# Kernel tuning notes

Hardware: AMD Instinct MI355X
Metric: run time of the kernel (lower is better)

## Reference

```python
import jax, jax.numpy as jnp
import numpy as np

B, N1, N2 = 2, 2048, 8192
IN_F, OUT_F = 128, 64
ALPHA = 0.2
NEG = -9e15


def setup_inputs() -> dict:
    key = jax.random.key(0)
    ks = jax.random.split(key, 8)
    stdv = 1.0 / np.sqrt(OUT_F)
    x = jax.random.normal(ks[0], (B, N2, IN_F), dtype=jnp.float32)
    adj = (jax.random.uniform(ks[1], (B, N1, N2)) < 0.05).astype(jnp.float32)
    u = lambda k, shp: jax.random.uniform(k, shp, minval=-stdv, maxval=stdv, dtype=jnp.float32)
    W2 = u(ks[2], (IN_F, OUT_F))
    W3 = u(ks[3], (OUT_F, OUT_F))
    a = u(ks[4], (2 * OUT_F, 1))
    a2 = u(ks[5], (2 * OUT_F, 1))
    word_ctx = u(ks[6], (OUT_F,))
    return {"x": x, "adj": adj, "W2": W2, "W3": W3, "a": a, "a2": a2, "word_ctx": word_ctx}


def reference(x, adj, W2, W3, a, a2, word_ctx):
    F_out = W2.shape[1]
    x4 = jnp.einsum('bnf,fo->bno', x, W2)            # [B, N2, F] node features for attention
    mask = adj > 0                                     # [B, N1, N2]
    # --- stage 1: edge-level attention over member nodes (softmax over N2) ---
    # pair score = leakyrelu([word_ctx, x4_j] @ a); independent of hyperedge index i
    a_q, a_x = a[:F_out, 0], a[F_out:, 0]
    s1 = jax.nn.leaky_relu(jnp.dot(word_ctx, a_q) + x4 @ a_x, ALPHA)  # [B, N2]
    e1 = jnp.where(mask, s1[:, None, :], NEG)          # [B, N1, N2]
    att_edge = jax.nn.softmax(e1, axis=2)
    edge = jnp.einsum('bij,bjf->bif', att_edge, x4)    # [B, N1, F]
    edge4 = jnp.einsum('bif,fo->bio', edge, W3)        # [B, N1, F]
    # --- stage 2: node-level attention over incident hyperedges (softmax over N1) ---
    a2_x, a2_e = a2[:F_out, 0], a2[F_out:, 0]
    s2 = jax.nn.leaky_relu((edge4 @ a2_e)[:, :, None] + (x4 @ a2_x)[:, None, :], ALPHA)  # [B, N1, N2]
    e2 = jnp.where(mask, s2, NEG)
    att_node = jax.nn.softmax(jnp.transpose(e2, (0, 2, 1)), axis=2)  # [B, N2, N1]
    node = jnp.einsum('bji,bif->bjf', att_node, edge4)               # [B, N2, F]
    return node, edge
```

## Files before the change

kernel.cpp:

```cpp
#include <hip/hip_runtime.h>
#include <stdint.h>

#define NB 2
#define N1 2048
#define N2 8192
#define INF_ 128
#define F 64
#define ALPHA 0.2f
#define CAP_E 640
#define CAP_N 192

__device__ __forceinline__ float bf2f(unsigned short u) {
    return __uint_as_float((unsigned int)u << 16);
}
__device__ __forceinline__ unsigned short f2bf(float f) {
    unsigned int u = __float_as_uint(f);
    u += 0x7FFF + ((u >> 16) & 1);
    return (unsigned short)(u >> 16);
}

__global__ __launch_bounds__(256) void k_mask_csr(
    const float4* __restrict__ adj4, uint64_t* __restrict__ bits,
    uint16_t* __restrict__ idxE, int* __restrict__ cntE)
{
    __shared__ uint64_t sBits[128];
    __shared__ uint16_t sIdx[CAP_E];
    __shared__ int      sCnt[4];
    int tid  = threadIdx.x;
    int lane = tid & 63;
    int w    = tid >> 6;
    int row  = blockIdx.x;
    int b    = row >> 11;

    const float4* ar = adj4 + (size_t)row * (N2 / 4) + (size_t)w * 512 + lane;
    float4 v[8];
    #pragma unroll
    for (int it = 0; it < 8; ++it) v[it] = ar[it * 64];
    int cnt = 0;
    #pragma unroll
    for (int it = 0; it < 8; ++it) {
        unsigned long long m0 = __ballot(v[it].x != 0.0f);
        unsigned long long m1 = __ballot(v[it].y != 0.0f);
        unsigned long long m2 = __ballot(v[it].z != 0.0f);
        unsigned long long m3 = __ballot(v[it].w != 0.0f);
        if (lane == 0) {
            uint64_t* o = &sBits[w * 32 + it * 4];
            o[0] = m0; o[1] = m1; o[2] = m2; o[3] = m3;
        }
        cnt += (int)__popcll(m0) + (int)__popcll(m1)
             + (int)__popcll(m2) + (int)__popcll(m3);
    }
    if (lane == 0) sCnt[w] = cnt;
    __syncthreads();

    int c0 = sCnt[0], c1 = sCnt[1], c2 = sCnt[2], c3 = sCnt[3];
    int base = (w > 0 ? c0 : 0) + (w > 1 ? c1 : 0) + (w > 2 ? c2 : 0);
    int total = c0 + c1 + c2 + c3;
    uint64_t lmask = (1ull << lane) - 1;
    #pragma unroll
    for (int k = 0; k < 32; ++k) {
        int wi = w * 32 + k;
        uint64_t m = sBits[wi];
        if ((m >> lane) & 1) {
            int pos = base + (int)__popcll(m & lmask);
            sIdx[pos] = (uint16_t)(((wi >> 2) << 8) + (lane << 2) + (wi & 3));
        }
        base += (int)__popcll(m);
    }
    int n = total;
    int padded = (n + 15) & ~15;
    if (padded > CAP_E) padded = CAP_E;
    if (w == 3) {
        uint16_t sent = (uint16_t)((NB - b) * N2);
        if (n + lane < padded) sIdx[n + lane] = sent;
    }
    __syncthreads();

    uint64_t* bw = bits + (size_t)row * (N2 / 64);
    if (tid < 128) bw[tid] = sBits[tid];
    const uint32_t* s32 = (const uint32_t*)sIdx;
    uint32_t* o32 = (uint32_t*)(idxE + (size_t)row * CAP_E);
    for (int d = tid; 2 * d < padded; d += 256) o32[d] = s32[d];
    if (tid == 0) cntE[row] = n;
}

__global__ __launch_bounds__(512) void k_x4(
    const float* __restrict__ x, const float* __restrict__ W2,
    const float* __restrict__ a, const float* __restrict__ a2,
    const float* __restrict__ wctx,
    uint16_t* __restrict__ y16, float* __restrict__ w1, float* __restrict__ q)
{
    __shared__ float  w2s[INF_ * F];
    __shared__ float4 xs4[64 * 32];
    int tid  = threadIdx.x;
    int lane = tid & 63;
    int w    = tid >> 6;

    for (int idx = tid; idx < INF_ * F; idx += 512) w2s[idx] = W2[idx];
    if (blockIdx.x == 0) {
        if (tid < F) y16[(size_t)NB * N2 * F + tid] = 0;
        if (tid == 0) w1[NB * N2] = 0.f;
    }
    {
        const float4* xg4 = (const float4*)(x + (size_t)blockIdx.x * 64 * INF_);
        int r  = tid >> 3;
        int c0 = (tid & 7) * 4;
        #pragma unroll
        for (int i = 0; i < 4; ++i)
            xs4[r * 32 + c0 + i] = xg4[r * 32 + c0 + i];
    }
    float cpart = wctx[lane] * a[lane];
    #pragma unroll
    for (int s = 32; s; s >>= 1) cpart += __shfl_xor(cpart, s);
    float ax  = a[64 + lane];
    float a2x = a2[lane];
    __syncthreads();

    float acc[8] = {0.f, 0.f, 0.f, 0.f, 0.f, 0.f, 0.f, 0.f};
    for (int k4 = 0; k4 < 32; ++k4) {
        float wk0 = w2s[(4 * k4 + 0) * F + lane];
        float wk1 = w2s[(4 * k4 + 1) * F + lane];
        float wk2 = w2s[(4 * k4 + 2) * F + lane];
        float wk3 = w2s[(4 * k4 + 3) * F + lane];
        #pragma unroll
        for (int r = 0; r < 8; ++r) {
            float4 xv = xs4[(8 * w + r) * 32 + k4];
            acc[r] = fmaf(xv.x, wk0, acc[r]);
            acc[r] = fmaf(xv.y, wk1, acc[r]);
            acc[r] = fmaf(xv.z, wk2, acc[r]);
            acc[r] = fmaf(xv.w, wk3, acc[r]);
        }
    }
    int row0 = blockIdx.x * 64 + 8 * w;
    #pragma unroll
    for (int r = 0; r < 8; ++r) {
        float acc_ = acc[r];
        float r1 = acc_ * ax, r2 = acc_ * a2x;
        #pragma unroll
        for (int s = 32; s; s >>= 1) { r1 += __shfl_xor(r1, s); r2 += __shfl_xor(r2, s); }
        float s1 = cpart + r1;
        s1 = fmaxf(s1, ALPHA * s1);
        float wv1 = __expf(s1);
        y16[(size_t)(row0 + r) * F + lane] = f2bf(wv1 * acc_);
        if (lane == 0) { w1[row0 + r] = wv1; q[row0 + r] = r2; }
    }
}

union SU {
    float w3[F * F];
    struct {
        uint16_t idxn[64][194];
        int      pre[4][64];
        int      cnt[64];
    } t;
};

__global__ __launch_bounds__(256) void kB2(
    const uint64_t* __restrict__ bits,
    uint16_t* __restrict__ idxN, int* __restrict__ cntN,
    const uint16_t* __restrict__ idxE, const int* __restrict__ cntE,
    const uint16_t* __restrict__ y16, const float* __restrict__ w1,
    const float* __restrict__ W3, const float* __restrict__ a2,
    float* __restrict__ out_edge, uint16_t* __restrict__ e16, float* __restrict__ p)
{
    __shared__ SU su;
    int tid  = threadIdx.x;
    int lane = tid & 63;
    int w    = tid >> 6;

    if (blockIdx.x < 256) {
        int b  = blockIdx.x >> 7;
        int jw = blockIdx.x & 127;
        const uint64_t Mtab[6] = {0x00000000FFFFFFFFull, 0x0000FFFF0000FFFFull,
                                  0x00FF00FF00FF00FFull, 0x0F0F0F0F0F0F0F0Full,
                                  0x3333333333333333ull, 0x5555555555555555ull};
        uint64_t wd[8];
        #pragma unroll
        for (int t = 0; t < 8; ++t) {
            int ib = w * 8 + t;
            uint64_t xv = bits[((size_t)(b * N1 + ib * 64 + lane)) * (N2 / 64) + jw];
            #pragma unroll
            for (int st = 0; st < 6; ++st) {
                int s = 32 >> st;
                uint64_t M = Mtab[st];
                uint64_t yy = (uint64_t)__shfl_xor((unsigned long long)xv, s);
                xv = ((lane & s) == 0) ? ((xv & M) | ((yy & M) << s))
                                       : ((xv & ~M) | ((yy & ~M) >> s));
            }
            wd[t] = xv;
        }
        int myc = 0;
        #pragma unroll
        for (int t = 0; t < 8; ++t) myc += (int)__popcll(wd[t]);
        su.t.pre[w][lane] = myc;
        __syncthreads();
        int c0 = su.t.pre[0][lane], c1 = su.t.pre[1][lane];
        int c2 = su.t.pre[2][lane], c3 = su.t.pre[3][lane];
        int base = (w > 0 ? c0 : 0) + (w > 1 ? c1 : 0) + (w > 2 ? c2 : 0);
        int total = c0 + c1 + c2 + c3;
        int n = total < CAP_N ? total : CAP_N;
        if (w == 0) su.t.cnt[lane] = n;

        uint16_t* sr = su.t.idxn[lane];
        int off = base;
        #pragma unroll
        for (int t = 0; t < 8; ++t) {
            uint64_t m = wd[t];
            int ibase = (w * 8 + t) << 6;
            while (m) {
                int ii = __builtin_ctzll(m); m &= m - 1;
                if (off < CAP_N) sr[off] = (uint16_t)(ibase + ii);
                ++off;
            }
        }
        int jp = jw * 64 + lane;
        int j  = ((jp >> 8) << 8) + ((jp & 63) << 2) + ((jp >> 6) & 3);
        int rowOut = b * N2 + j;
        if (w == 3) {
            int padded = (n + 15) & ~15;
            if (padded > CAP_N) padded = CAP_N;
            uint16_t sent = (uint16_t)((NB - b) * N1);
            for (int o = n; o < padded; ++o) sr[o] = sent;
            cntN[rowOut] = n;
        }
        __syncthreads();
        int jbase = b * N2 + ((jw >> 2) << 8) + (jw & 3);
        for (int rr = 0; rr < 16; ++rr) {
            int r = w * 16 + rr;
            int n_r = su.t.cnt[r];
            int padded_r = (n_r + 15) & ~15;
            if (padded_r > CAP_N) padded_r = CAP_N;
            int rowOut_r = jbase + r * 4;
            uint32_t* dst = (uint32_t*)(idxN + (size_t)rowOut_r * CAP_N);
            const uint32_t* src = (const uint32_t*)su.t.idxn[r];
            for (int d = lane; 2 * d < padded_r; d += 64) dst[d] = src[d];
        }
    } else {
        for (int idx = tid; idx < F * F; idx += blockDim.x) su.w3[idx] = W3[idx];
        if (blockIdx.x == 256 && tid == 0) p[NB * N1] = -1e30f;
        __syncthreads();
        int g    = lane >> 4;
        int sub  = lane & 15;
        float a2e = a2[64 + lane];
        int row = ((blockIdx.x - 256) * 256 + tid) >> 6;
        if (row >= NB * N1) return;
        int b = row >> 11;
        const ushort4* yb = (const ushort4*)y16 + (size_t)b * N2 * 16;
        const float*   w1b = w1 + (size_t)b * N2;
        const uint16_t* ix = idxE + (size_t)row * CAP_E;
        int n = cntE[row];
        int padded = (n + 15) & ~15;
        if (padded > CAP_E) padded = CAP_E;
        float4 acc = make_float4(0.f, 0.f, 0.f, 0.f);
        float zl = 0.f, zl4 = 0.f;
        int t = 0;
        for (; t + 64 <= padded; t += 64) {
            int myj = ix[t + lane];
            zl += w1b[myj];
            #pragma unroll
            for (int s = 0; s < 16; ++s) {
                int jv = __shfl(myj, 4 * s + g);
                ushort4 v = yb[(size_t)jv * 16 + sub];
                acc.x += bf2f(v.x); acc.y += bf2f(v.y);
                acc.z += bf2f(v.z); acc.w += bf2f(v.w);
            }
        }
        for (; t < padded; t += 16) {
            int myj = ix[t + (lane & 15)];
            zl4 += w1b[myj];
            #pragma unroll
            for (int s = 0; s < 4; ++s) {
                int jv = __shfl(myj, 4 * s + g);
                ushort4 v = yb[(size_t)jv * 16 + sub];
                acc.x += bf2f(v.x); acc.y += bf2f(v.y);
                acc.z += bf2f(v.z); acc.w += bf2f(v.w);
            }
        }
        #pragma unroll
        for (int s2 = 16; s2 <= 32; s2 <<= 1) {
            acc.x += __shfl_xor(acc.x, s2);
            acc.y += __shfl_xor(acc.y, s2);
            acc.z += __shfl_xor(acc.z, s2);
            acc.w += __shfl_xor(acc.w, s2);
        }
        float zc = zl + 0.25f * zl4;
        #pragma unroll
        for (int s2 = 32; s2; s2 >>= 1) zc += __shfl_xor(zc, s2);
        float inv = 1.f / zc;
        float4 ev4 = make_float4(acc.x * inv, acc.y * inv, acc.z * inv, acc.w * inv);
        if (lane < 16) ((float4*)out_edge)[(size_t)row * 16 + sub] = ev4;
        float e0 = __shfl(ev4.x, lane >> 2);
        float e1 = __shfl(ev4.y, lane >> 2);
        float e2 = __shfl(ev4.z, lane >> 2);
        float e3 = __shfl(ev4.w, lane >> 2);
        int c = lane & 3;
        float ev = (c == 0) ? e0 : (c == 1) ? e1 : (c == 2) ? e2 : e3;
        float acc4 = 0.f;
        #pragma unroll 8
        for (int gg = 0; gg < 64; ++gg) acc4 += __shfl(ev, gg) * su.w3[gg * F + lane];
        e16[(size_t)row * F + lane] = f2bf(acc4);
        float r = acc4 * a2e;
        #pragma unroll
        for (int s2 = 32; s2; s2 >>= 1) r += __shfl_xor(r, s2);
        if (lane == 0) p[row] = r;
    }
}

__global__ __launch_bounds__(256) void kE(
    const uint16_t* __restrict__ idxN, const int* __restrict__ cntN,
    const uint16_t* __restrict__ e16, const float* __restrict__ p,
    const float* __restrict__ q, float* __restrict__ out_node)
{
    int lane = threadIdx.x & 63;
    int g    = lane >> 4;
    int sub  = lane & 15;
    int gw = (blockIdx.x * blockDim.x + threadIdx.x) >> 6;
    int nw = (gridDim.x * blockDim.x) >> 6;
    for (int row = gw; row < NB * N2; row += nw) {
        int b = row >> 13;
        const ushort4* eb = (const ushort4*)e16 + (size_t)b * N1 * 16;
        const float*   pb = p + b * N1;
        const uint16_t* ix = idxN + (size_t)row * CAP_N;
        float qj = q[row];
        int n = cntN[row];
        int padded = (n + 15) & ~15;
        if (padded > CAP_N) padded = CAP_N;
        float4 acc = make_float4(0.f, 0.f, 0.f, 0.f);
        float zl = 0.f, zl4 = 0.f;
        int t = 0;
        for (; t + 64 <= padded; t += 64) {
            int myi = ix[t + lane];
            float sc = pb[myi] + qj;
            sc = fmaxf(sc, ALPHA * sc);
            float wl = __expf(sc);
            zl += wl;
            #pragma unroll
            for (int s = 0; s < 16; ++s) {
                int iv   = __shfl(myi, 4 * s + g);
                float wv = __shfl(wl,  4 * s + g);
                ushort4 v = eb[(size_t)iv * 16 + sub];
                acc.x = fmaf(wv, bf2f(v.x), acc.x);
                acc.y = fmaf(wv, bf2f(v.y), acc.y);
                acc.z = fmaf(wv, bf2f(v.z), acc.z);
                acc.w = fmaf(wv, bf2f(v.w), acc.w);
            }
        }
        for (; t < padded; t += 16) {
            int myi = ix[t + (lane & 15)];
            float sc = pb[myi] + qj;
            sc = fmaxf(sc, ALPHA * sc);
            float wl = __expf(sc);
            zl4 += wl;
            #pragma unroll
            for (int s = 0; s < 4; ++s) {
                int iv   = __shfl(myi, 4 * s + g);
                float wv = __shfl(wl,  4 * s + g);
                ushort4 v = eb[(size_t)iv * 16 + sub];
                acc.x = fmaf(wv, bf2f(v.x), acc.x);
                acc.y = fmaf(wv, bf2f(v.y), acc.y);
                acc.z = fmaf(wv, bf2f(v.z), acc.z);
                acc.w = fmaf(wv, bf2f(v.w), acc.w);
            }
        }
        #pragma unroll
        for (int s2 = 16; s2 <= 32; s2 <<= 1) {
            acc.x += __shfl_xor(acc.x, s2);
            acc.y += __shfl_xor(acc.y, s2);
            acc.z += __shfl_xor(acc.z, s2);
            acc.w += __shfl_xor(acc.w, s2);
        }
        float zc = zl + 0.25f * zl4;
        #pragma unroll
        for (int s2 = 32; s2; s2 >>= 1) zc += __shfl_xor(zc, s2);
        float inv = 1.f / zc;
        if (lane < 16) {
            float4 o = make_float4(acc.x * inv, acc.y * inv, acc.z * inv, acc.w * inv);
            ((float4*)out_node)[(size_t)row * 16 + sub] = o;
        }
    }
}

extern "C" void kernel_launch(void* const* d_in, const int* in_sizes, int n_in,
                              void* d_out, int out_size, void* d_ws, size_t ws_size,
                              hipStream_t stream)
{
    const float* x    = (const float*)d_in[0];
    const float* adj  = (const float*)d_in[1];
    const float* W2   = (const float*)d_in[2];
    const float* W3   = (const float*)d_in[3];
    const float* a    = (const float*)d_in[4];
    const float* a2   = (const float*)d_in[5];
    const float* wctx = (const float*)d_in[6];

    float* out      = (float*)d_out;
    float* node_out = out;
    float* edge_out = out + (size_t)NB * N2 * F;

    char* basep = (char*)d_ws;
    size_t o = 0;
    uint16_t* y16 = (uint16_t*)(basep + o);
    o += (size_t)(NB * N2 + 1) * F * 2;        o = (o + 255) & ~(size_t)255;
    float* w1 = (float*)(basep + o);
    o += (size_t)(NB * N2 + 4) * 4;            o = (o + 255) & ~(size_t)255;
    float* q = (float*)(basep + o);
    o += (size_t)NB * N2 * 4;                  o = (o + 255) & ~(size_t)255;
    uint16_t* e16 = (uint16_t*)(basep + o);
    o += (size_t)(NB * N1 + 1) * F * 2;        o = (o + 255) & ~(size_t)255;
    float* p = (float*)(basep + o);
    o += (size_t)(NB * N1 + 4) * 4;            o = (o + 255) & ~(size_t)255;
    uint64_t* bits = (uint64_t*)(basep + o);
    o += (size_t)NB * N1 * (N2 / 64) * 8;
    int* cntE = (int*)(basep + o);             o += (size_t)NB * N1 * 4;
    int* cntN = (int*)(basep + o);             o += (size_t)NB * N2 * 4;
    uint16_t* idxE = (uint16_t*)(basep + o);   o += (size_t)NB * N1 * CAP_E * 2;
    uint16_t* idxN = (uint16_t*)(basep + o);

    hipLaunchKernelGGL(k_mask_csr, dim3(NB * N1), dim3(256), 0, stream,
                       (const float4*)adj, bits, idxE, cntE);
    hipLaunchKernelGGL(k_x4, dim3(NB * N2 / 64), dim3(512), 0, stream,
                       x, W2, a, a2, wctx, y16, w1, q);
    hipLaunchKernelGGL(kB2, dim3(1280), dim3(256), 0, stream,
                       bits, idxN, cntN, idxE, cntE, y16, w1, W3, a2,
                       edge_out, e16, p);
    hipLaunchKernelGGL(kE, dim3(4096), dim3(256), 0, stream,
                       idxN, cntN, e16, p, q, node_out);
}
```

Measured before the change: 97.36 us.

## Split each hyperedge row across four wavefronts with shared-memory reduction

The edge-aggregation branch of kB2 now gives each hyperedge row a whole 256-thread block instead of one wavefront. The four waves stride over the row's member list in 16-entry chunks, and their partial feature sums and softmax denominators are combined through shared memory. Wave 0 then applies the W3 projection and writes the outputs. This raises parallelism for long rows and shortens the per-row latency chain. The cost is four times as many blocks, a block-wide barrier, each block reloading W3 into shared memory, and three of the four waves sitting idle during the projection.

```diff
diff --git a/kernel.cpp b/kernel.cpp
--- a/kernel.cpp
+++ b/kernel.cpp
@@ -147,7 +147,11 @@
 }
 
 union SU {
-    float w3[F * F];
+    struct {
+        float  w3[F * F];
+        float4 red[4][16];
+        float  zred[4];
+    } d;
     struct {
         uint16_t idxn[64][194];
         int      pre[4][64];
@@ -236,36 +240,21 @@
             for (int d = lane; 2 * d < padded_r; d += 64) dst[d] = src[d];
         }
     } else {
-        for (int idx = tid; idx < F * F; idx += blockDim.x) su.w3[idx] = W3[idx];
+        for (int idx = tid; idx < F * F; idx += 256) su.d.w3[idx] = W3[idx];
         if (blockIdx.x == 256 && tid == 0) p[NB * N1] = -1e30f;
-        __syncthreads();
-        int g    = lane >> 4;
-        int sub  = lane & 15;
-        float a2e = a2[64 + lane];
-        int row = ((blockIdx.x - 256) * 256 + tid) >> 6;
-        if (row >= NB * N1) return;
+        int row = blockIdx.x - 256;
         int b = row >> 11;
         const ushort4* yb = (const ushort4*)y16 + (size_t)b * N2 * 16;
         const float*   w1b = w1 + (size_t)b * N2;
         const uint16_t* ix = idxE + (size_t)row * CAP_E;
+        int g    = lane >> 4;
+        int sub  = lane & 15;
         int n = cntE[row];
         int padded = (n + 15) & ~15;
         if (padded > CAP_E) padded = CAP_E;
         float4 acc = make_float4(0.f, 0.f, 0.f, 0.f);
-        float zl = 0.f, zl4 = 0.f;
-        int t = 0;
-        for (; t + 64 <= padded; t += 64) {
-            int myj = ix[t + lane];
-            zl += w1b[myj];
-            #pragma unroll
-            for (int s = 0; s < 16; ++s) {
-                int jv = __shfl(myj, 4 * s + g);
-                ushort4 v = yb[(size_t)jv * 16 + sub];
-                acc.x += bf2f(v.x); acc.y += bf2f(v.y);
-                acc.z += bf2f(v.z); acc.w += bf2f(v.w);
-            }
-        }
-        for (; t < padded; t += 16) {
+        float zl4 = 0.f;
+        for (int t = 16 * w; t < padded; t += 64) {
             int myj = ix[t + (lane & 15)];
             zl4 += w1b[myj];
             #pragma unroll
@@ -283,26 +272,40 @@
             acc.z += __shfl_xor(acc.z, s2);
             acc.w += __shfl_xor(acc.w, s2);
         }
-        float zc = zl + 0.25f * zl4;
+        float zc = 0.25f * zl4;
         #pragma unroll
         for (int s2 = 32; s2; s2 >>= 1) zc += __shfl_xor(zc, s2);
-        float inv = 1.f / zc;
-        float4 ev4 = make_float4(acc.x * inv, acc.y * inv, acc.z * inv, acc.w * inv);
-        if (lane < 16) ((float4*)out_edge)[(size_t)row * 16 + sub] = ev4;
-        float e0 = __shfl(ev4.x, lane >> 2);
-        float e1 = __shfl(ev4.y, lane >> 2);
-        float e2 = __shfl(ev4.z, lane >> 2);
-        float e3 = __shfl(ev4.w, lane >> 2);
-        int c = lane & 3;
-        float ev = (c == 0) ? e0 : (c == 1) ? e1 : (c == 2) ? e2 : e3;
-        float acc4 = 0.f;
-        #pragma unroll 8
-        for (int gg = 0; gg < 64; ++gg) acc4 += __shfl(ev, gg) * su.w3[gg * F + lane];
-        e16[(size_t)row * F + lane] = f2bf(acc4);
-        float r = acc4 * a2e;
-        #pragma unroll
-        for (int s2 = 32; s2; s2 >>= 1) r += __shfl_xor(r, s2);
-        if (lane == 0) p[row] = r;
+        if (lane < 16) su.d.red[w][sub] = acc;
+        if (lane == 0) su.d.zred[w] = zc;
+        __syncthreads();
+        if (w == 0) {
+            float4 A0 = su.d.red[0][sub], A1 = su.d.red[1][sub];
+            float4 A2 = su.d.red[2][sub], A3 = su.d.red[3][sub];
+            float4 As = make_float4((A0.x + A1.x) + (A2.x + A3.x),
+                                    (A0.y + A1.y) + (A2.y + A3.y),
+                                    (A0.z + A1.z) + (A2.z + A3.z),
+                                    (A0.w + A1.w) + (A2.w + A3.w));
+            float z = (su.d.zred[0] + su.d.zred[1]) + (su.d.zred[2] + su.d.zred[3]);
+            float inv = 1.f / z;
+            float4 ev4 = make_float4(As.x * inv, As.y * inv, As.z * inv, As.w * inv);
+            if (lane < 16) ((float4*)out_edge)[(size_t)row * 16 + sub] = ev4;
+            float e0 = __shfl(ev4.x, lane >> 2);
+            float e1 = __shfl(ev4.y, lane >> 2);
+            float e2 = __shfl(ev4.z, lane >> 2);
+            float e3 = __shfl(ev4.w, lane >> 2);
+            int c = lane & 3;
+            float ev = (c == 0) ? e0 : (c == 1) ? e1 : (c == 2) ? e2 : e3;
+            float a2e = a2[64 + lane];
+            float acc4 = 0.f;
+            #pragma unroll 8
+            for (int gg = 0; gg < 64; ++gg)
+                acc4 += __shfl(ev, gg) * su.d.w3[gg * F + lane];
+            e16[(size_t)row * F + lane] = f2bf(acc4);
+            float r = acc4 * a2e;
+            #pragma unroll
+            for (int s2 = 32; s2; s2 >>= 1) r += __shfl_xor(r, s2);
+            if (lane == 0) p[row] = r;
+        }
     }
 }
 
@@ -419,7 +422,7 @@
                        (const float4*)adj, bits, idxE, cntE);
     hipLaunchKernelGGL(k_x4, dim3(NB * N2 / 64), dim3(512), 0, stream,
                        x, W2, a, a2, wctx, y16, w1, q);
-    hipLaunchKernelGGL(kB2, dim3(1280), dim3(256), 0, stream,
+    hipLaunchKernelGGL(kB2, dim3(256 + NB * N1), dim3(256), 0, stream,
                        bits, idxN, cntN, idxE, cntE, y16, w1, W3, a2,
                        edge_out, e16, p);
     hipLaunchKernelGGL(kE, dim3(4096), dim3(256), 0, stream,
```

Measured after the change: 103.3 us. +6.1%, slower.

## Fuse node-CSR transpose into x4 kernel; split edge aggregation; widen gathers to 16B

Applied to the files above, without the earlier changes.

Moves the bit-matrix transpose that builds the node CSR out of the edge-aggregation kernel and into the x4 projection kernel, running it as extra 512-thread blocks there. Edge aggregation becomes its own kernel, so it no longer waits on the transpose work. Both gather loops (edge and node) now load 8 bf16 values per lane as uint4 instead of 4 as ushort4, halving the number of gather instructions and shuffles. Risks are changed occupancy from the larger shared-memory union, an extra launch boundary, and more registers per lane.

```diff
diff --git a/kernel.cpp b/kernel.cpp
--- a/kernel.cpp
+++ b/kernel.cpp
@@ -18,6 +18,8 @@
     u += 0x7FFF + ((u >> 16) & 1);
     return (unsigned short)(u >> 16);
 }
+__device__ __forceinline__ float blo(unsigned int d) { return __uint_as_float(d << 16); }
+__device__ __forceinline__ float bhi(unsigned int d) { return __uint_as_float(d & 0xFFFF0000u); }
 
 __global__ __launch_bounds__(256) void k_mask_csr(
     const float4* __restrict__ adj4, uint64_t* __restrict__ bits,
@@ -84,100 +86,88 @@
     if (tid == 0) cntE[row] = n;
 }
 
-__global__ __launch_bounds__(512) void k_x4(
+union XU {
+    struct { float w2s[INF_ * F]; float4 xs4[64 * 32]; } x;
+    struct {
+        uint16_t idxn[64][194];
+        int      pre[8][64];
+        int      cnt[64];
+    } t;
+};
+
+__global__ __launch_bounds__(512) void k_x4t(
     const float* __restrict__ x, const float* __restrict__ W2,
     const float* __restrict__ a, const float* __restrict__ a2,
     const float* __restrict__ wctx,
-    uint16_t* __restrict__ y16, float* __restrict__ w1, float* __restrict__ q)
+    uint16_t* __restrict__ y16, float* __restrict__ w1, float* __restrict__ q,
+    const uint64_t* __restrict__ bits,
+    uint16_t* __restrict__ idxN, int* __restrict__ cntN)
 {
-    __shared__ float  w2s[INF_ * F];
-    __shared__ float4 xs4[64 * 32];
+    __shared__ XU su;
     int tid  = threadIdx.x;
     int lane = tid & 63;
     int w    = tid >> 6;
 
-    for (int idx = tid; idx < INF_ * F; idx += 512) w2s[idx] = W2[idx];
-    if (blockIdx.x == 0) {
-        if (tid < F) y16[(size_t)NB * N2 * F + tid] = 0;
-        if (tid == 0) w1[NB * N2] = 0.f;
-    }
-    {
-        const float4* xg4 = (const float4*)(x + (size_t)blockIdx.x * 64 * INF_);
-        int r  = tid >> 3;
-        int c0 = (tid & 7) * 4;
-        #pragma unroll
-        for (int i = 0; i < 4; ++i)
-            xs4[r * 32 + c0 + i] = xg4[r * 32 + c0 + i];
-    }
-    float cpart = wctx[lane] * a[lane];
-    #pragma unroll
-    for (int s = 32; s; s >>= 1) cpart += __shfl_xor(cpart, s);
-    float ax  = a[64 + lane];
-    float a2x = a2[lane];
-    __syncthreads();
-
-    float acc[8] = {0.f, 0.f, 0.f, 0.f, 0.f, 0.f, 0.f, 0.f};
-    for (int k4 = 0; k4 < 32; ++k4) {
-        float wk0 = w2s[(4 * k4 + 0) * F + lane];
-        float wk1 = w2s[(4 * k4 + 1) * F + lane];
-        float wk2 = w2s[(4 * k4 + 2) * F + lane];
-        float wk3 = w2s[(4 * k4 + 3) * F + lane];
+    if (blockIdx.x < 256) {
+        for (int idx = tid; idx < INF_ * F; idx += 512) su.x.w2s[idx] = W2[idx];
+        if (blockIdx.x == 0) {
+            if (tid < F) y16[(size_t)NB * N2 * F + tid] = 0;
+            if (tid == 0) w1[NB * N2] = 0.f;
+        }
+        {
+            const float4* xg4 = (const float4*)(x + (size_t)blockIdx.x * 64 * INF_);
+            int r  = tid >> 3;
+            int c0 = (tid & 7) * 4;
+            #pragma unroll
+            for (int i = 0; i < 4; ++i)
+                su.x.xs4[r * 32 + c0 + i] = xg4[r * 32 + c0 + i];
+        }
+        float cpart = wctx[lane] * a[lane];
+        #pragma unroll
+        for (int s = 32; s; s >>= 1) cpart += __shfl_xor(cpart, s);
+        float ax  = a[64 + lane];
+        float a2x = a2[lane];
+        __syncthreads();
+
+        float acc[8] = {0.f, 0.f, 0.f, 0.f, 0.f, 0.f, 0.f, 0.f};
+        for (int k4 = 0; k4 < 32; ++k4) {
+            float wk0 = su.x.w2s[(4 * k4 + 0) * F + lane];
+            float wk1 = su.x.w2s[(4 * k4 + 1) * F + lane];
+            float wk2 = su.x.w2s[(4 * k4 + 2) * F + lane];
+            float wk3 = su.x.w2s[(4 * k4 + 3) * F + lane];
+            #pragma unroll
+            for (int r = 0; r < 8; ++r) {
+                float4 xv = su.x.xs4[(8 * w + r) * 32 + k4];
+                acc[r] = fmaf(xv.x, wk0, acc[r]);
+                acc[r] = fmaf(xv.y, wk1, acc[r]);
+                acc[r] = fmaf(xv.z, wk2, acc[r]);
+                acc[r] = fmaf(xv.w, wk3, acc[r]);
+            }
+        }
+        int row0 = blockIdx.x * 64 + 8 * w;
         #pragma unroll
         for (int r = 0; r < 8; ++r) {
-            float4 xv = xs4[(8 * w + r) * 32 + k4];
-            acc[r] = fmaf(xv.x, wk0, acc[r]);
-            acc[r] = fmaf(xv.y, wk1, acc[r]);
-            acc[r] = fmaf(xv.z, wk2, acc[r]);
-            acc[r] = fmaf(xv.w, wk3, acc[r]);
-        }
-    }
-    int row0 = blockIdx.x * 64 + 8 * w;
-    #pragma unroll
-    for (int r = 0; r < 8; ++r) {
-        float acc_ = acc[r];
-        float r1 = acc_ * ax, r2 = acc_ * a2x;
-        #pragma unroll
-        for (int s = 32; s; s >>= 1) { r1 += __shfl_xor(r1, s); r2 += __shfl_xor(r2, s); }
-        float s1 = cpart + r1;
-        s1 = fmaxf(s1, ALPHA * s1);
-        float wv1 = __expf(s1);
-        y16[(size_t)(row0 + r) * F + lane] = f2bf(wv1 * acc_);
-        if (lane == 0) { w1[row0 + r] = wv1; q[row0 + r] = r2; }
-    }
-}
-
-union SU {
-    float w3[F * F];
-    struct {
-        uint16_t idxn[64][194];
-        int      pre[4][64];
-        int      cnt[64];
-    } t;
-};
-
-__global__ __launch_bounds__(256) void kB2(
-    const uint64_t* __restrict__ bits,
-    uint16_t* __restrict__ idxN, int* __restrict__ cntN,
-    const uint16_t* __restrict__ idxE, const int* __restrict__ cntE,
-    const uint16_t* __restrict__ y16, const float* __restrict__ w1,
-    const float* __restrict__ W3, const float* __restrict__ a2,
-    float* __restrict__ out_edge, uint16_t* __restrict__ e16, float* __restrict__ p)
-{
-    __shared__ SU su;
-    int tid  = threadIdx.x;
-    int lane = tid & 63;
-    int w    = tid >> 6;
-
-    if (blockIdx.x < 256) {
-        int b  = blockIdx.x >> 7;
-        int jw = blockIdx.x & 127;
+            float acc_ = acc[r];
+            float r1 = acc_ * ax, r2 = acc_ * a2x;
+            #pragma unroll
+            for (int s = 32; s; s >>= 1) { r1 += __shfl_xor(r1, s); r2 += __shfl_xor(r2, s); }
+            float s1 = cpart + r1;
+            s1 = fmaxf(s1, ALPHA * s1);
+            float wv1 = __expf(s1);
+            y16[(size_t)(row0 + r) * F + lane] = f2bf(wv1 * acc_);
+            if (lane == 0) { w1[row0 + r] = wv1; q[row0 + r] = r2; }
+        }
+    } else {
+        int blk = blockIdx.x - 256;
+        int b  = blk >> 7;
+        int jw = blk & 127;
         const uint64_t Mtab[6] = {0x00000000FFFFFFFFull, 0x0000FFFF0000FFFFull,
                                   0x00FF00FF00FF00FFull, 0x0F0F0F0F0F0F0F0Full,
                                   0x3333333333333333ull, 0x5555555555555555ull};
-        uint64_t wd[8];
-        #pragma unroll
-        for (int t = 0; t < 8; ++t) {
-            int ib = w * 8 + t;
+        uint64_t wd[4];
+        #pragma unroll
+        for (int t = 0; t < 4; ++t) {
+            int ib = w * 4 + t;
             uint64_t xv = bits[((size_t)(b * N1 + ib * 64 + lane)) * (N2 / 64) + jw];
             #pragma unroll
             for (int st = 0; st < 6; ++st) {
@@ -191,22 +181,25 @@
         }
         int myc = 0;
         #pragma unroll
-        for (int t = 0; t < 8; ++t) myc += (int)__popcll(wd[t]);
+        for (int t = 0; t < 4; ++t) myc += (int)__popcll(wd[t]);
         su.t.pre[w][lane] = myc;
         __syncthreads();
-        int c0 = su.t.pre[0][lane], c1 = su.t.pre[1][lane];
-        int c2 = su.t.pre[2][lane], c3 = su.t.pre[3][lane];
-        int base = (w > 0 ? c0 : 0) + (w > 1 ? c1 : 0) + (w > 2 ? c2 : 0);
-        int total = c0 + c1 + c2 + c3;
+        int base = 0, total = 0;
+        #pragma unroll
+        for (int ww = 0; ww < 8; ++ww) {
+            int c = su.t.pre[ww][lane];
+            if (ww < w) base += c;
+            total += c;
+        }
         int n = total < CAP_N ? total : CAP_N;
         if (w == 0) su.t.cnt[lane] = n;
 
         uint16_t* sr = su.t.idxn[lane];
         int off = base;
         #pragma unroll
-        for (int t = 0; t < 8; ++t) {
+        for (int t = 0; t < 4; ++t) {
             uint64_t m = wd[t];
-            int ibase = (w * 8 + t) << 6;
+            int ibase = (w * 4 + t) << 6;
             while (m) {
                 int ii = __builtin_ctzll(m); m &= m - 1;
                 if (off < CAP_N) sr[off] = (uint16_t)(ibase + ii);
@@ -216,7 +209,7 @@
         int jp = jw * 64 + lane;
         int j  = ((jp >> 8) << 8) + ((jp & 63) << 2) + ((jp >> 6) & 3);
         int rowOut = b * N2 + j;
-        if (w == 3) {
+        if (w == 7) {
             int padded = (n + 15) & ~15;
             if (padded > CAP_N) padded = CAP_N;
             uint16_t sent = (uint16_t)((NB - b) * N1);
@@ -225,8 +218,8 @@
         }
         __syncthreads();
         int jbase = b * N2 + ((jw >> 2) << 8) + (jw & 3);
-        for (int rr = 0; rr < 16; ++rr) {
-            int r = w * 16 + rr;
+        for (int rr = 0; rr < 8; ++rr) {
+            int r = w * 8 + rr;
             int n_r = su.t.cnt[r];
             int padded_r = (n_r + 15) & ~15;
             if (padded_r > CAP_N) padded_r = CAP_N;
@@ -235,75 +228,93 @@
             const uint32_t* src = (const uint32_t*)su.t.idxn[r];
             for (int d = lane; 2 * d < padded_r; d += 64) dst[d] = src[d];
         }
-    } else {
-        for (int idx = tid; idx < F * F; idx += blockDim.x) su.w3[idx] = W3[idx];
-        if (blockIdx.x == 256 && tid == 0) p[NB * N1] = -1e30f;
-        __syncthreads();
-        int g    = lane >> 4;
-        int sub  = lane & 15;
-        float a2e = a2[64 + lane];
-        int row = ((blockIdx.x - 256) * 256 + tid) >> 6;
-        if (row >= NB * N1) return;
-        int b = row >> 11;
-        const ushort4* yb = (const ushort4*)y16 + (size_t)b * N2 * 16;
-        const float*   w1b = w1 + (size_t)b * N2;
-        const uint16_t* ix = idxE + (size_t)row * CAP_E;
-        int n = cntE[row];
-        int padded = (n + 15) & ~15;
-        if (padded > CAP_E) padded = CAP_E;
-        float4 acc = make_float4(0.f, 0.f, 0.f, 0.f);
-        float zl = 0.f, zl4 = 0.f;
-        int t = 0;
-        for (; t + 64 <= padded; t += 64) {
-            int myj = ix[t + lane];
-            zl += w1b[myj];
-            #pragma unroll
-            for (int s = 0; s < 16; ++s) {
-                int jv = __shfl(myj, 4 * s + g);
-                ushort4 v = yb[(size_t)jv * 16 + sub];
-                acc.x += bf2f(v.x); acc.y += bf2f(v.y);
-                acc.z += bf2f(v.z); acc.w += bf2f(v.w);
-            }
-        }
-        for (; t < padded; t += 16) {
-            int myj = ix[t + (lane & 15)];
-            zl4 += w1b[myj];
-            #pragma unroll
-            for (int s = 0; s < 4; ++s) {
-                int jv = __shfl(myj, 4 * s + g);
-                ushort4 v = yb[(size_t)jv * 16 + sub];
-                acc.x += bf2f(v.x); acc.y += bf2f(v.y);
-                acc.z += bf2f(v.z); acc.w += bf2f(v.w);
-            }
-        }
-        #pragma unroll
-        for (int s2 = 16; s2 <= 32; s2 <<= 1) {
-            acc.x += __shfl_xor(acc.x, s2);
-            acc.y += __shfl_xor(acc.y, s2);
-            acc.z += __shfl_xor(acc.z, s2);
-            acc.w += __shfl_xor(acc.w, s2);
-        }
-        float zc = zl + 0.25f * zl4;
-        #pragma unroll
-        for (int s2 = 32; s2; s2 >>= 1) zc += __shfl_xor(zc, s2);
-        float inv = 1.f / zc;
-        float4 ev4 = make_float4(acc.x * inv, acc.y * inv, acc.z * inv, acc.w * inv);
-        if (lane < 16) ((float4*)out_edge)[(size_t)row * 16 + sub] = ev4;
-        float e0 = __shfl(ev4.x, lane >> 2);
-        float e1 = __shfl(ev4.y, lane >> 2);
-        float e2 = __shfl(ev4.z, lane >> 2);
-        float e3 = __shfl(ev4.w, lane >> 2);
-        int c = lane & 3;
-        float ev = (c == 0) ? e0 : (c == 1) ? e1 : (c == 2) ? e2 : e3;
-        float acc4 = 0.f;
-        #pragma unroll 8
-        for (int gg = 0; gg < 64; ++gg) acc4 += __shfl(ev, gg) * su.w3[gg * F + lane];
-        e16[(size_t)row * F + lane] = f2bf(acc4);
-        float r = acc4 * a2e;
-        #pragma unroll
-        for (int s2 = 32; s2; s2 >>= 1) r += __shfl_xor(r, s2);
-        if (lane == 0) p[row] = r;
-    }
+    }
+}
+
+__global__ __launch_bounds__(256) void kD(
+    const uint16_t* __restrict__ idxE, const int* __restrict__ cntE,
+    const uint16_t* __restrict__ y16, const float* __restrict__ w1,
+    const float* __restrict__ W3, const float* __restrict__ a2,
+    float* __restrict__ out_edge, uint16_t* __restrict__ e16, float* __restrict__ p)
+{
+    __shared__ float  w3s[F * F];
+    __shared__ float4 scr4[4][16];
+    int tid  = threadIdx.x;
+    int lane = tid & 63;
+    int w    = tid >> 6;
+    for (int idx = tid; idx < F * F; idx += 256) w3s[idx] = W3[idx];
+    if (blockIdx.x == 0 && tid == 0) p[NB * N1] = -1e30f;
+    __syncthreads();
+    int g   = lane >> 3;
+    int sub = lane & 7;
+    int row = (blockIdx.x * 256 + tid) >> 6;
+    int b = row >> 11;
+    const uint4* yb = (const uint4*)y16 + (size_t)b * N2 * 8;
+    const float* w1b = w1 + (size_t)b * N2;
+    const uint16_t* ix = idxE + (size_t)row * CAP_E;
+    int n = cntE[row];
+    int padded = (n + 15) & ~15;
+    if (padded > CAP_E) padded = CAP_E;
+    float4 aA = make_float4(0.f, 0.f, 0.f, 0.f);
+    float4 aB = make_float4(0.f, 0.f, 0.f, 0.f);
+    float zl = 0.f, zl4 = 0.f;
+    int t = 0;
+    for (; t + 64 <= padded; t += 64) {
+        int myj = ix[t + lane];
+        zl += w1b[myj];
+        #pragma unroll
+        for (int s = 0; s < 8; ++s) {
+            int jv = __shfl(myj, 8 * s + g);
+            uint4 v = yb[(size_t)jv * 8 + sub];
+            aA.x += blo(v.x); aA.y += bhi(v.x);
+            aA.z += blo(v.y); aA.w += bhi(v.y);
+            aB.x += blo(v.z); aB.y += bhi(v.z);
+            aB.z += blo(v.w); aB.w += bhi(v.w);
+        }
+    }
+    for (; t < padded; t += 16) {
+        int myj = ix[t + (lane & 15)];
+        zl4 += w1b[myj];
+        #pragma unroll
+        for (int s = 0; s < 2; ++s) {
+            int jv = __shfl(myj, 8 * s + g);
+            uint4 v = yb[(size_t)jv * 8 + sub];
+            aA.x += blo(v.x); aA.y += bhi(v.x);
+            aA.z += blo(v.y); aA.w += bhi(v.y);
+            aB.x += blo(v.z); aB.y += bhi(v.z);
+            aB.z += blo(v.w); aB.w += bhi(v.w);
+        }
+    }
+    #pragma unroll
+    for (int s2 = 8; s2 <= 32; s2 <<= 1) {
+        aA.x += __shfl_xor(aA.x, s2); aA.y += __shfl_xor(aA.y, s2);
+        aA.z += __shfl_xor(aA.z, s2); aA.w += __shfl_xor(aA.w, s2);
+        aB.x += __shfl_xor(aB.x, s2); aB.y += __shfl_xor(aB.y, s2);
+        aB.z += __shfl_xor(aB.z, s2); aB.w += __shfl_xor(aB.w, s2);
+    }
+    float zc = zl + 0.25f * zl4;
+    #pragma unroll
+    for (int s2 = 32; s2; s2 >>= 1) zc += __shfl_xor(zc, s2);
+    float inv = 1.f / zc;
+    float4 evA = make_float4(aA.x * inv, aA.y * inv, aA.z * inv, aA.w * inv);
+    float4 evB = make_float4(aB.x * inv, aB.y * inv, aB.z * inv, aB.w * inv);
+    if (lane < 8) {
+        float4* o4 = (float4*)out_edge + (size_t)row * 16;
+        o4[2 * lane]     = evA;
+        o4[2 * lane + 1] = evB;
+        scr4[w][2 * lane]     = evA;
+        scr4[w][2 * lane + 1] = evB;
+    }
+    float ev = ((const float*)scr4[w])[lane];
+    float a2e = a2[64 + lane];
+    float acc4 = 0.f;
+    #pragma unroll 8
+    for (int gg = 0; gg < 64; ++gg) acc4 += __shfl(ev, gg) * w3s[gg * F + lane];
+    e16[(size_t)row * F + lane] = f2bf(acc4);
+    float r = acc4 * a2e;
+    #pragma unroll
+    for (int s2 = 32; s2; s2 >>= 1) r += __shfl_xor(r, s2);
+    if (lane == 0) p[row] = r;
 }
 
 __global__ __launch_bounds__(256) void kE(
@@ -312,20 +323,21 @@
     const float* __restrict__ q, float* __restrict__ out_node)
 {
     int lane = threadIdx.x & 63;
-    int g    = lane >> 4;
-    int sub  = lane & 15;
+    int g   = lane >> 3;
+    int sub = lane & 7;
     int gw = (blockIdx.x * blockDim.x + threadIdx.x) >> 6;
     int nw = (gridDim.x * blockDim.x) >> 6;
     for (int row = gw; row < NB * N2; row += nw) {
         int b = row >> 13;
-        const ushort4* eb = (const ushort4*)e16 + (size_t)b * N1 * 16;
-        const float*   pb = p + b * N1;
+        const uint4*  eb = (const uint4*)e16 + (size_t)b * N1 * 8;
+        const float*  pb = p + b * N1;
         const uint16_t* ix = idxN + (size_t)row * CAP_N;
         float qj = q[row];
         int n = cntN[row];
         int padded = (n + 15) & ~15;
         if (padded > CAP_N) padded = CAP_N;
-        float4 acc = make_float4(0.f, 0.f, 0.f, 0.f);
+        float4 aA = make_float4(0.f, 0.f, 0.f, 0.f);
+        float4 aB = make_float4(0.f, 0.f, 0.f, 0.f);
         float zl = 0.f, zl4 = 0.f;
         int t = 0;
         for (; t + 64 <= padded; t += 64) {
@@ -335,14 +347,14 @@
             float wl = __expf(sc);
             zl += wl;
             #pragma unroll
-            for (int s = 0; s < 16; ++s) {
-                int iv   = __shfl(myi, 4 * s + g);
-                float wv = __shfl(wl,  4 * s + g);
-                ushort4 v = eb[(size_t)iv * 16 + sub];
-                acc.x = fmaf(wv, bf2f(v.x), acc.x);
-                acc.y = fmaf(wv, bf2f(v.y), acc.y);
-                acc.z = fmaf(wv, bf2f(v.z), acc.z);
-                acc.w = fmaf(wv, bf2f(v.w), acc.w);
+            for (int s = 0; s < 8; ++s) {
+                int iv   = __shfl(myi, 8 * s + g);
+                float wv = __shfl(wl,  8 * s + g);
+                uint4 v = eb[(size_t)iv * 8 + sub];
+                aA.x = fmaf(wv, blo(v.x), aA.x); aA.y = fmaf(wv, bhi(v.x), aA.y);
+                aA.z = fmaf(wv, blo(v.y), aA.z); aA.w = fmaf(wv, bhi(v.y), aA.w);
+                aB.x = fmaf(wv, blo(v.z), aB.x); aB.y = fmaf(wv, bhi(v.z), aB.y);
+                aB.z = fmaf(wv, blo(v.w), aB.z); aB.w = fmaf(wv, bhi(v.w), aB.w);
             }
         }
         for (; t < padded; t += 16) {
@@ -352,30 +364,31 @@
             float wl = __expf(sc);
             zl4 += wl;
             #pragma unroll
-            for (int s = 0; s < 4; ++s) {
-                int iv   = __shfl(myi, 4 * s + g);
-                float wv = __shfl(wl,  4 * s + g);
-                ushort4 v = eb[(size_t)iv * 16 + sub];
-                acc.x = fmaf(wv, bf2f(v.x), acc.x);
-                acc.y = fmaf(wv, bf2f(v.y), acc.y);
-                acc.z = fmaf(wv, bf2f(v.z), acc.z);
-                acc.w = fmaf(wv, bf2f(v.w), acc.w);
+            for (int s = 0; s < 2; ++s) {
+                int iv   = __shfl(myi, 8 * s + g);
+                float wv = __shfl(wl,  8 * s + g);
+                uint4 v = eb[(size_t)iv * 8 + sub];
+                aA.x = fmaf(wv, blo(v.x), aA.x); aA.y = fmaf(wv, bhi(v.x), aA.y);
+                aA.z = fmaf(wv, blo(v.y), aA.z); aA.w = fmaf(wv, bhi(v.y), aA.w);
+                aB.x = fmaf(wv, blo(v.z), aB.x); aB.y = fmaf(wv, bhi(v.z), aB.y);
+                aB.z = fmaf(wv, blo(v.w), aB.z); aB.w = fmaf(wv, bhi(v.w), aB.w);
             }
         }
         #pragma unroll
-        for (int s2 = 16; s2 <= 32; s2 <<= 1) {
-            acc.x += __shfl_xor(acc.x, s2);
-            acc.y += __shfl_xor(acc.y, s2);
-            acc.z += __shfl_xor(acc.z, s2);
-            acc.w += __shfl_xor(acc.w, s2);
+        for (int s2 = 8; s2 <= 32; s2 <<= 1) {
+            aA.x += __shfl_xor(aA.x, s2); aA.y += __shfl_xor(aA.y, s2);
+            aA.z += __shfl_xor(aA.z, s2); aA.w += __shfl_xor(aA.w, s2);
+            aB.x += __shfl_xor(aB.x, s2); aB.y += __shfl_xor(aB.y, s2);
+            aB.z += __shfl_xor(aB.z, s2); aB.w += __shfl_xor(aB.w, s2);
         }
         float zc = zl + 0.25f * zl4;
         #pragma unroll
         for (int s2 = 32; s2; s2 >>= 1) zc += __shfl_xor(zc, s2);
         float inv = 1.f / zc;
-        if (lane < 16) {
-            float4 o = make_float4(acc.x * inv, acc.y * inv, acc.z * inv, acc.w * inv);
-            ((float4*)out_node)[(size_t)row * 16 + sub] = o;
+        if (lane < 8) {
+            float4* o4 = (float4*)out_node + (size_t)row * 16;
+            o4[2 * lane]     = make_float4(aA.x * inv, aA.y * inv, aA.z * inv, aA.w * inv);
+            o4[2 * lane + 1] = make_float4(aB.x * inv, aB.y * inv, aB.z * inv, aB.w * inv);
         }
     }
 }
@@ -417,11 +430,10 @@
 
     hipLaunchKernelGGL(k_mask_csr, dim3(NB * N1), dim3(256), 0, stream,
                        (const float4*)adj, bits, idxE, cntE);
-    hipLaunchKernelGGL(k_x4, dim3(NB * N2 / 64), dim3(512), 0, stream,
-                       x, W2, a, a2, wctx, y16, w1, q);
-    hipLaunchKernelGGL(kB2, dim3(1280), dim3(256), 0, stream,
-                       bits, idxN, cntN, idxE, cntE, y16, w1, W3, a2,
-                       edge_out, e16, p);
+    hipLaunchKernelGGL(k_x4t, dim3(512), dim3(512), 0, stream,
+                       x, W2, a, a2, wctx, y16, w1, q, bits, idxN, cntN);
+    hipLaunchKernelGGL(kD, dim3(NB * N1 / 4), dim3(256), 0, stream,
+                       idxE, cntE, y16, w1, W3, a2, edge_out, e16, p);
     hipLaunchKernelGGL(kE, dim3(4096), dim3(256), 0, stream,
                        idxN, cntN, e16, p, q, node_out);
 }
```

After: 88.08 us. 1.11x faster.
